# Kernel optimization log

Hardware: AMD Instinct MI355X
Metric: run time of the kernel (lower is better)

## Reference

```python
import jax, jax.numpy as jnp
import numpy as np

DN = ('NCDHW', 'OIDHW', 'NCDHW')
HEAD_COUNT = 8
LN_EPS = 1e-5


def _dwpw(x, dw_w, dw_b, pw_w, pw_b):
    # depthwise 3x3x3 conv (groups=C) followed by pointwise 1x1x1 conv, both with bias
    cin = x.shape[1]
    y = jax.lax.conv_general_dilated(x, dw_w, (1, 1, 1), [(1, 1), (1, 1), (1, 1)],
                                     dimension_numbers=DN, feature_group_count=cin)
    y = y + dw_b[None, :, None, None, None]
    y = jax.lax.conv_general_dilated(y, pw_w, (1, 1, 1), [(0, 0), (0, 0), (0, 0)],
                                     dimension_numbers=DN)
    return y + pw_b[None, :, None, None, None]


def setup_inputs() -> dict:
    key = jax.random.key(0)
    ks = iter(jax.random.split(key, 64))
    C, KC, VC = 256, 256, 256
    n, t, h, w = 4, 16, 28, 28
    d = {}
    d['input_rgb'] = jax.random.normal(next(ks), (n, C, t, h, w), dtype=jnp.float32)
    d['input_flow'] = jax.random.normal(next(ks), (n, C, t, h, w), dtype=jnp.float32)

    def conv_params(cin, cout, pfx):
        d[pfx + '_dw_w'] = jax.random.normal(next(ks), (cin, 1, 3, 3, 3), dtype=jnp.float32) * 0.05
        d[pfx + '_dw_b'] = jnp.zeros((cin,), dtype=jnp.float32)
        d[pfx + '_pw_w'] = jax.random.normal(next(ks), (cout, cin, 1, 1, 1), dtype=jnp.float32) * 0.05
        d[pfx + '_pw_b'] = jnp.zeros((cout,), dtype=jnp.float32)

    for s in ('rgb', 'flow'):
        for p, cout in (('k', KC), ('q', KC), ('v', VC)):
            conv_params(C, cout, f'{s}_{p}')
    conv_params(2 * VC, 2 * C, 'rp')
    return d


def reference(input_rgb, input_flow,
              rgb_k_dw_w, rgb_k_dw_b, rgb_k_pw_w, rgb_k_pw_b,
              rgb_q_dw_w, rgb_q_dw_b, rgb_q_pw_w, rgb_q_pw_b,
              rgb_v_dw_w, rgb_v_dw_b, rgb_v_pw_w, rgb_v_pw_b,
              flow_k_dw_w, flow_k_dw_b, flow_k_pw_w, flow_k_pw_b,
              flow_q_dw_w, flow_q_dw_b, flow_q_pw_w, flow_q_pw_b,
              flow_v_dw_w, flow_v_dw_b, flow_v_pw_w, flow_v_pw_b,
              rp_dw_w, rp_dw_b, rp_pw_w, rp_pw_b):
    n, C, t, h, w = input_rgb.shape
    S = t * h * w
    fused = jnp.concatenate([input_rgb, input_flow], axis=1)  # [n, 2C, t, h, w]

    def proj(x, dw_w, dw_b, pw_w, pw_b):
        return _dwpw(x, dw_w, dw_b, pw_w, pw_b).reshape(n, -1, S)

    keys = jnp.concatenate([proj(input_rgb, rgb_k_dw_w, rgb_k_dw_b, rgb_k_pw_w, rgb_k_pw_b),
                            proj(input_flow, flow_k_dw_w, flow_k_dw_b, flow_k_pw_w, flow_k_pw_b)], axis=1)
    queries = jnp.concatenate([proj(input_rgb, rgb_q_dw_w, rgb_q_dw_b, rgb_q_pw_w, rgb_q_pw_b),
                               proj(input_flow, flow_q_dw_w, flow_q_dw_b, flow_q_pw_w, flow_q_pw_b)], axis=1)
    values = jnp.concatenate([proj(input_rgb, rgb_v_dw_w, rgb_v_dw_b, rgb_v_pw_w, rgb_v_pw_b),
                              proj(input_flow, flow_v_dw_w, flow_v_dw_b, flow_v_pw_w, flow_v_pw_b)], axis=1)

    H = HEAD_COUNT
    hk = keys.shape[1] // H
    hv = values.shape[1] // H
    K = jax.nn.softmax(keys.reshape(n, H, hk, S), axis=3)      # softmax over sequence
    Q = jax.nn.softmax(queries.reshape(n, H, hk, S), axis=2)   # softmax over head channels
    V = values.reshape(n, H, hv, S)

    ctx = jnp.einsum('nhks,nhvs->nhkv', K, V)                   # [n,H,hk,hv]
    att = jnp.einsum('nhkv,nhks->nhvs', ctx, Q)                 # [n,H,hv,S]
    aggregated = att.reshape(n, H * hv, t, h, w)                # [n, 2*VC, t, h, w]

    rep = _dwpw(aggregated, rp_dw_w, rp_dw_b, rp_pw_w, rp_pw_b)
    x = rep + fused
    # f.layer_norm(x, x.size()): normalize over the ENTIRE tensor, no affine
    m = x.mean()
    v = x.var()
    return (x - m) / jnp.sqrt(v + LN_EPS)
```

## Files before the change

kernel.cpp:

```cpp
#include <hip/hip_runtime.h>
#include <math.h>


constexpr int NN = 4;
constexpr int C1 = 256;
constexpr int C2 = 512;
constexpr int TT = 16;
constexpr int SP = TT * 28 * 28;
constexpr long long NB = (long long)NN * C2 * SP;
constexpr int HEADS = 8;
constexpr int CTX_CHUNKS = 7;
constexpr int STATS_PARTS = 98 * 4 * 4;
constexpr double TOTAL_ELEMS = (double)NB;

typedef __attribute__((ext_vector_type(8))) short bf16x8;
typedef __attribute__((ext_vector_type(4))) short bf16x4;
typedef __attribute__((ext_vector_type(4))) float f32x4;

__device__ __forceinline__ short f2bf(float f)
{
    unsigned u = __float_as_uint(f);
    unsigned r = u + 0x7FFFu + ((u >> 16) & 1u);
    return (short)(r >> 16);
}
__device__ __forceinline__ float bf2f(short s)
{
    return __uint_as_float(((unsigned)(unsigned short)s) << 16);
}

__device__ __forceinline__ float4 loadvec4(const float* p)
{
    return *(const float4*)p;
}
__device__ __forceinline__ float4 loadvec4(const short* p)
{
    bf16x4 v = *(const bf16x4*)p;
    return (float4){bf2f(v[0]), bf2f(v[1]), bf2f(v[2]), bf2f(v[3])};
}

__device__ __forceinline__ void gload16(const short* g, short* l)
{
    __builtin_amdgcn_global_load_lds(
        (const __attribute__((address_space(1))) unsigned int*)g,
        (__attribute__((address_space(3))) unsigned int*)l,
        16, 0, 0);
}

__global__ __launch_bounds__(256)
void wcvt_kernel(const float* __restrict__ w0, const float* __restrict__ w1,
                 const float* __restrict__ w2, const float* __restrict__ w3,
                 const float* __restrict__ w4, const float* __restrict__ w5,
                 const float* __restrict__ w6, short* __restrict__ out)
{
    int i = blockIdx.x * 256 + threadIdx.x;
    if (i >= 655360) return;
    const float* src; int off;
    if (i < 393216) {
        int seg = i >> 16; off = i & 65535;
        src = seg == 0 ? w0 : seg == 1 ? w1 : seg == 2 ? w2
            : seg == 3 ? w3 : seg == 4 ? w4 : w5;
    } else { src = w6; off = i - 393216; }
    out[i] = f2bf(src[off]);
}

template<typename IT, int NSET>
__global__ __launch_bounds__(256)
void dwv_kernel(const IT* __restrict__ in,
                const float* __restrict__ w0c, const float* __restrict__ b0c,
                short* __restrict__ o0,
                const float* __restrict__ w1c, const float* __restrict__ b1c,
                short* __restrict__ o1,
                const float* __restrict__ w2c, const float* __restrict__ b2c,
                short* __restrict__ o2, int Cin)
{
    const int split = blockIdx.x, c = blockIdx.y, n = blockIdx.z;
    const int t0 = split * 8, t1 = t0 + 8;
    const int zs = (t0 - 1 > 0) ? t0 - 1 : 0;
    const int ze = (t1 < 15) ? t1 : 15;
    __shared__ float tile[2][900];
    const int tid = threadIdx.x;
    const size_t ibase = ((size_t)(n * Cin + c)) * TT * 784;
    const IT* inp = in + ibase;

    const float* wp[3] = {w0c, w1c, w2c};
    const float* bp[3] = {b0c, b1c, b2c};
    short* op[3] = {o0, o1, o2};
    float w[NSET][27], bv[NSET];
#pragma unroll
    for (int g = 0; g < NSET; ++g) {
#pragma unroll
        for (int i = 0; i < 27; ++i) w[g][i] = wp[g][c * 27 + i];
        bv[g] = bp[g][c];
    }

    for (int i = tid; i < 1800; i += 256) ((float*)tile)[i] = 0.f;

    const bool act = tid < 196;
    const int pos = tid * 4;
    const int hh = pos / 28, ww = pos - hh * 28;
    const int ladr = (hh + 1) * 30 + ww + 1;
    const int rbase = hh * 30 + ww;

    float4 preg = {0.f, 0.f, 0.f, 0.f};
    if (act) preg = loadvec4(inp + (size_t)zs * 784 + pos);

    float a0[NSET][4], a1[NSET][4], a2[NSET][4];
#pragma unroll
    for (int g = 0; g < NSET; ++g)
#pragma unroll
        for (int k = 0; k < 4; ++k) { a0[g][k] = bv[g]; a1[g][k] = bv[g]; a2[g][k] = bv[g]; }

    for (int z = zs; z <= ze; ++z) {
        float* tb = tile[z & 1];
        __syncthreads();
        if (act) {
            tb[ladr] = preg.x; tb[ladr + 1] = preg.y;
            tb[ladr + 2] = preg.z; tb[ladr + 3] = preg.w;
            if (z < ze) preg = loadvec4(inp + (size_t)(z + 1) * 784 + pos);
        }
        __syncthreads();
        if (act) {
            float v[3][6];
#pragma unroll
            for (int r = 0; r < 3; ++r)
#pragma unroll
                for (int j = 0; j < 6; ++j)
                    v[r][j] = tb[rbase + r * 30 + j];
#pragma unroll
            for (int g = 0; g < NSET; ++g)
#pragma unroll
                for (int dh = 0; dh < 3; ++dh)
#pragma unroll
                    for (int dw = 0; dw < 3; ++dw) {
                        const float wa = w[g][18 + dh * 3 + dw];
                        const float wb = w[g][9 + dh * 3 + dw];
                        const float wc2 = w[g][dh * 3 + dw];
#pragma unroll
                        for (int k = 0; k < 4; ++k) {
                            const float val = v[dh][k + dw];
                            a0[g][k] += val * wa;
                            a1[g][k] += val * wb;
                            a2[g][k] += val * wc2;
                        }
                    }
            if (z - 1 >= t0) {
#pragma unroll
                for (int g = 0; g < NSET; ++g) {
                    bf16x4 pk;
#pragma unroll
                    for (int k = 0; k < 4; ++k) pk[k] = f2bf(a0[g][k]);
                    *(bf16x4*)&op[g][ibase + (size_t)(z - 1) * 784 + pos] = pk;
                }
            }
#pragma unroll
            for (int g = 0; g < NSET; ++g)
#pragma unroll
                for (int k = 0; k < 4; ++k) {
                    a0[g][k] = a1[g][k]; a1[g][k] = a2[g][k]; a2[g][k] = bv[g];
                }
        }
    }
    if (act && ze >= t0 && ze < t1) {
#pragma unroll
        for (int g = 0; g < NSET; ++g) {
            bf16x4 pk;
#pragma unroll
            for (int k = 0; k < 4; ++k) pk[k] = f2bf(a0[g][k]);
            *(bf16x4*)&op[g][ibase + (size_t)ze * 784 + pos] = pk;
        }
    }
}

template<int MODE>
__global__ __launch_bounds__(256)
void pw_mfma_kernel(const short* __restrict__ Wb, const float* __restrict__ bias,
                    const short* __restrict__ act, short* __restrict__ outB,
                    float* __restrict__ outF, const float* __restrict__ rgb,
                    const float* __restrict__ flow, double* __restrict__ partials,
                    int Cin, size_t nStride, size_t cStride, int chOff)
{
    __shared__ short smem[17408];
    short* lA = smem;
    short* Bs = smem + 8192;
    const int tid = threadIdx.x;
    const int w = tid >> 6, lane = tid & 63;
    const int s0 = blockIdx.x * 128;
    const int m0 = blockIdx.y * 128;
    const int n = blockIdx.z;
    const short* aSrc = Wb + (size_t)m0 * Cin;
    const short* bSrc = act + (size_t)n * Cin * SP;
    f32x4 acc[4][4];
#pragma unroll
    for (int i = 0; i < 4; ++i)
#pragma unroll
        for (int j = 0; j < 4; ++j)
            acc[i][j] = (f32x4){0.f, 0.f, 0.f, 0.f};
    const int lrow = lane >> 3, lslot = lane & 7;
    const int wr = w >> 1, wc = w & 1;
    const int kg = tid >> 4, scb = tid & 15;

    for (int kt = 0; kt < Cin; kt += 64) {
#pragma unroll
        for (int cc = 0; cc < 4; ++cc) {
            const int chunk = w * 4 + cc;
            const int row = chunk * 8 + lrow;
            const int ss = lslot ^ (row & 7);
            gload16(aSrc + (size_t)row * Cin + kt + ss * 8, &lA[chunk * 512]);
        }
        bf16x8 breg[4];
#pragma unroll
        for (int r = 0; r < 4; ++r)
            breg[r] = *(const bf16x8*)(bSrc + (size_t)(kt + kg * 4 + r) * SP + s0 + scb * 8);
#pragma unroll
        for (int j = 0; j < 8; ++j) {
            bf16x4 pk;
#pragma unroll
            for (int r = 0; r < 4; ++r) pk[r] = breg[r][j];
            const int srow = scb * 8 + j;
            const int slot = (kg >> 1) ^ (scb & 7);
            *(bf16x4*)&Bs[srow * 72 + slot * 8 + (kg & 1) * 4] = pk;
        }
        __syncthreads();
#pragma unroll
        for (int kf = 0; kf < 2; ++kf) {
            bf16x8 af[4], bfr[4];
            const int kb = kf * 4 + (lane >> 4);
#pragma unroll
            for (int i = 0; i < 4; ++i) {
                const int row = wr * 64 + i * 16 + (lane & 15);
                af[i] = *(const bf16x8*)&lA[row * 64 + ((kb ^ (row & 7)) << 3)];
            }
#pragma unroll
            for (int j = 0; j < 4; ++j) {
                const int srow = wc * 64 + j * 16 + (lane & 15);
                bfr[j] = *(const bf16x8*)&Bs[srow * 72 + ((kb ^ ((srow >> 3) & 7)) << 3)];
            }
#pragma unroll
            for (int i = 0; i < 4; ++i)
#pragma unroll
                for (int j = 0; j < 4; ++j)
                    acc[i][j] = __builtin_amdgcn_mfma_f32_16x16x32_bf16(
                        af[i], bfr[j], acc[i][j], 0, 0, 0);
        }
        __syncthreads();
    }

    if constexpr (MODE == 0) {
        short* ep = smem;
#pragma unroll
        for (int i = 0; i < 4; ++i) {
            const int mloc = wr * 64 + i * 16 + (lane >> 4) * 4;
#pragma unroll
            for (int j = 0; j < 4; ++j) {
                const int sloc = wc * 64 + j * 16 + (lane & 15);
#pragma unroll
                for (int r = 0; r < 4; ++r)
                    ep[(mloc + r) * 136 + sloc] =
                        f2bf(acc[i][j][r] + bias[m0 + mloc + r]);
            }
        }
        __syncthreads();
        short* op = outB + (size_t)n * nStride;
#pragma unroll
        for (int cc = 0; cc < 8; ++cc) {
            const int idx = tid + cc * 256;
            const int mloc = idx >> 4, ch = idx & 15;
            bf16x8 v = *(const bf16x8*)&ep[mloc * 136 + ch * 8];
            *(bf16x8*)&op[(size_t)(chOff + m0 + mloc) * cStride + s0 + ch * 8] = v;
        }
    } else if constexpr (MODE == 1) {
        short* ep = smem;
#pragma unroll
        for (int i = 0; i < 4; ++i) {
            const int mb = wr * 64 + i * 16 + (lane >> 4) * 4;
#pragma unroll
            for (int j = 0; j < 4; ++j) {
                const int sloc = wc * 64 + j * 16 + (lane & 15);
                bf16x4 pk;
#pragma unroll
                for (int r = 0; r < 4; ++r)
                    pk[r] = f2bf(acc[i][j][r] + bias[m0 + mb + r]);
                *(bf16x4*)&ep[sloc * 136 + mb] = pk;
            }
        }
        __syncthreads();
#pragma unroll
        for (int cc = 0; cc < 8; ++cc) {
            const int idx = tid + cc * 256;
            const int sloc = idx >> 4, ch = idx & 15;
            bf16x8 v = *(const bf16x8*)&ep[sloc * 136 + ch * 8];
            *(bf16x8*)&outB[((size_t)n * SP + s0 + sloc) * 512 + chOff + m0 + ch * 8] = v;
        }
    } else {
        float* ep = (float*)smem;
        float* xp = outF + (size_t)n * C2 * SP;
        const float* rbase = (m0 < 256)
            ? rgb + ((size_t)n * 256 + m0) * SP
            : flow + ((size_t)n * 256 + (m0 - 256)) * SP;
        double ls = 0.0, lss = 0.0;
#pragma unroll
        for (int p = 0; p < 2; ++p) {
            if (p) __syncthreads();
            if (wr == p) {
#pragma unroll
                for (int i = 0; i < 4; ++i) {
                    const int mloc = i * 16 + (lane >> 4) * 4;
#pragma unroll
                    for (int j = 0; j < 4; ++j) {
                        const int sloc = wc * 64 + j * 16 + (lane & 15);
#pragma unroll
                        for (int r = 0; r < 4; ++r)
                            ep[(mloc + r) * 132 + sloc] =
                                acc[i][j][r] + bias[m0 + p * 64 + mloc + r];
                    }
                }
            }
            __syncthreads();
#pragma unroll
            for (int cc = 0; cc < 8; ++cc) {
                const int idx = tid + cc * 256;
                const int row = idx >> 5, ch = idx & 31;
                const int m = m0 + p * 64 + row;
                float4 a = *(const float4*)&ep[row * 132 + ch * 4];
                float4 rs = *(const float4*)&rbase[(size_t)(p * 64 + row) * SP + s0 + ch * 4];
                float4 x;
                x.x = a.x + rs.x; x.y = a.y + rs.y;
                x.z = a.z + rs.z; x.w = a.w + rs.w;
                *(float4*)&xp[(size_t)m * SP + s0 + ch * 4] = x;
                ls += (double)x.x + (double)x.y + (double)x.z + (double)x.w;
                lss += (double)x.x * x.x + (double)x.y * x.y +
                       (double)x.z * x.z + (double)x.w * x.w;
            }
        }
        __shared__ double s1[256], s2[256];
        s1[tid] = ls; s2[tid] = lss;
        __syncthreads();
        for (int st = 128; st > 0; st >>= 1) {
            if (tid < st) { s1[tid] += s1[tid + st]; s2[tid] += s2[tid + st]; }
            __syncthreads();
        }
        if (tid == 0) {
            const size_t bid = ((size_t)blockIdx.z * gridDim.y + blockIdx.y) *
                               gridDim.x + blockIdx.x;
            partials[2 * bid] = s1[0];
            partials[2 * bid + 1] = s2[0];
        }
    }
}

__global__ __launch_bounds__(256)
void row_stats_kernel(const short* __restrict__ K, float2* __restrict__ st)
{
    const short* p = K + (size_t)blockIdx.x * SP;
    __shared__ float sm[4];
    __shared__ float bc;
    const int tid = threadIdx.x, wv = tid >> 6, ln = tid & 63;
    float m = -1e30f;
    for (int c = tid; c < SP / 8; c += 256) {
        bf16x8 v = *(const bf16x8*)(p + c * 8);
#pragma unroll
        for (int j = 0; j < 8; ++j) m = fmaxf(m, bf2f(v[j]));
    }
    for (int o = 32; o; o >>= 1) m = fmaxf(m, __shfl_down(m, o, 64));
    if (ln == 0) sm[wv] = m;
    __syncthreads();
    if (tid == 0) bc = fmaxf(fmaxf(sm[0], sm[1]), fmaxf(sm[2], sm[3]));
    __syncthreads();
    m = bc;
    float sum = 0.f;
    for (int c = tid; c < SP / 8; c += 256) {
        bf16x8 v = *(const bf16x8*)(p + c * 8);
#pragma unroll
        for (int j = 0; j < 8; ++j) sum += __expf(bf2f(v[j]) - m);
    }
    for (int o = 32; o; o >>= 1) sum += __shfl_down(sum, o, 64);
    __syncthreads();
    if (ln == 0) sm[wv] = sum;
    __syncthreads();
    if (tid == 0) {
        float tot = sm[0] + sm[1] + sm[2] + sm[3];
        st[blockIdx.x] = (float2){m, 1.f / tot};
    }
}

__global__ __launch_bounds__(256)
void ctx_mfma_kernel(const short* __restrict__ Kb, const short* __restrict__ Vb,
                     const float2* __restrict__ stats, float* __restrict__ part)
{
    const int chunk = blockIdx.x, nh = blockIdx.y;
    const short* Kp = Kb + (size_t)nh * 64 * SP;
    const short* Vp = Vb + (size_t)nh * 64 * SP;
    __shared__ short lK[64 * 256];
    __shared__ short lV[64 * 256];
    const int tid = threadIdx.x;
    const int w = tid >> 6, lane = tid & 63;
    const int wr = w >> 1, wc = w & 1;
    f32x4 acc[2][2];
#pragma unroll
    for (int i = 0; i < 2; ++i)
#pragma unroll
        for (int j = 0; j < 2; ++j)
            acc[i][j] = (f32x4){0.f, 0.f, 0.f, 0.f};

    float km8[8], ki8[8];
#pragma unroll
    for (int ps = 0; ps < 8; ++ps) {
        float2 s = stats[nh * 64 + (tid >> 5) + ps * 8];
        km8[ps] = s.x; ki8[ps] = s.y;
    }

    for (int sub = 0; sub < 7; ++sub) {
        const int sOff = chunk * 1792 + sub * 256;
#pragma unroll
        for (int cc = 0; cc < 8; ++cc) {
            const int ch = w * 8 + cc;
            const int row = ch * 2 + (lane >> 5);
            const int sc = lane & 31;
            gload16(Vp + (size_t)row * SP + sOff + ((sc ^ (row & 7)) << 3),
                    &lV[ch * 512]);
        }
#pragma unroll
        for (int ps = 0; ps < 8; ++ps) {
            const int row = (tid >> 5) + ps * 8;
            const int sc = tid & 31;
            bf16x8 kv = *(const bf16x8*)(Kp + (size_t)row * SP + sOff + sc * 8);
            bf16x8 ev;
#pragma unroll
            for (int j = 0; j < 8; ++j)
                ev[j] = f2bf(__expf(bf2f(kv[j]) - km8[ps]) * ki8[ps]);
            *(bf16x8*)&lK[row * 256 + ((sc ^ (row & 7)) << 3)] = ev;
        }
        __syncthreads();
#pragma unroll
        for (int ks = 0; ks < 8; ++ks) {
            const int kb = ks * 4 + (lane >> 4);
            bf16x8 ak[2], bv[2];
#pragma unroll
            for (int i = 0; i < 2; ++i) {
                const int rk = wr * 32 + i * 16 + (lane & 15);
                ak[i] = *(const bf16x8*)&lK[rk * 256 + ((kb ^ (rk & 7)) << 3)];
            }
#pragma unroll
            for (int j = 0; j < 2; ++j) {
                const int rv = wc * 32 + j * 16 + (lane & 15);
                bv[j] = *(const bf16x8*)&lV[rv * 256 + ((kb ^ (rv & 7)) << 3)];
            }
#pragma unroll
            for (int i = 0; i < 2; ++i)
#pragma unroll
                for (int j = 0; j < 2; ++j)
                    acc[i][j] = __builtin_amdgcn_mfma_f32_16x16x32_bf16(
                        ak[i], bv[j], acc[i][j], 0, 0, 0);
        }
        __syncthreads();
    }
    float* op = part + ((size_t)nh * CTX_CHUNKS + chunk) * 4096;
#pragma unroll
    for (int i = 0; i < 2; ++i)
#pragma unroll
        for (int j = 0; j < 2; ++j)
#pragma unroll
            for (int r = 0; r < 4; ++r) {
                const int k = wr * 32 + i * 16 + (lane >> 4) * 4 + r;
                const int v = wc * 32 + j * 16 + (lane & 15);
                op[k * 64 + v] = acc[i][j][r];
            }
}

__global__ __launch_bounds__(256)
void ctx_reduce_kernel(const float* __restrict__ part, float* __restrict__ ctx)
{
    const int nh = blockIdx.x;
    for (int e = threadIdx.x; e < 4096; e += 256) {
        float s = 0.f;
        for (int c = 0; c < CTX_CHUNKS; ++c)
            s += part[((size_t)nh * CTX_CHUNKS + c) * 4096 + e];
        ctx[(size_t)nh * 4096 + e] = s;
    }
}

__global__ __launch_bounds__(256)
void att_kernel(const float* __restrict__ ctx, const short* __restrict__ Qb,
                short* __restrict__ out)
{
    const int nh = blockIdx.y;
    const int n = nh >> 3, h = nh & 7;
    const int s0 = blockIdx.x * 64;
    const float* cp = ctx + (size_t)nh * 4096;
    __shared__ short lC[64 * 64];
    __shared__ short lQ[64 * 64];
    __shared__ float red[64][4];
    __shared__ short lO[64 * 72];
    const int tid = threadIdx.x;
    const int w = tid >> 6, lane = tid & 63;

#pragma unroll
    for (int u = 0; u < 2; ++u) {
        const int si = (tid >> 6) + u * 4;
        const int v = tid & 63;
        bf16x8 pk;
#pragma unroll
        for (int j = 0; j < 8; ++j) pk[j] = f2bf(cp[(si * 8 + j) * 64 + v]);
        *(bf16x8*)&lC[v * 64 + ((si ^ (v & 7)) << 3)] = pk;
    }
    const int sq = tid >> 2, qpart = tid & 3;
    const short* Qrow = Qb + ((size_t)n * SP + s0 + sq) * 512 + h * 64 + qpart * 16;
    bf16x8 q0 = *(const bf16x8*)(Qrow);
    bf16x8 q1 = *(const bf16x8*)(Qrow + 8);
    float e[16];
    float mx = -1e30f;
#pragma unroll
    for (int j = 0; j < 8; ++j) {
        e[j] = bf2f(q0[j]); e[8 + j] = bf2f(q1[j]);
        mx = fmaxf(mx, fmaxf(e[j], e[8 + j]));
    }
    red[sq][qpart] = mx;
    __syncthreads();
    mx = fmaxf(fmaxf(red[sq][0], red[sq][1]), fmaxf(red[sq][2], red[sq][3]));
    float sum = 0.f;
#pragma unroll
    for (int j = 0; j < 16; ++j) { e[j] = __expf(e[j] - mx); sum += e[j]; }
    __syncthreads();
    red[sq][qpart] = sum;
    __syncthreads();
    const float sinv = 1.f / (red[sq][0] + red[sq][1] + red[sq][2] + red[sq][3]);
    bf16x8 p0, p1;
#pragma unroll
    for (int j = 0; j < 8; ++j) {
        p0[j] = f2bf(e[j] * sinv);
        p1[j] = f2bf(e[8 + j] * sinv);
    }
    *(bf16x8*)&lQ[sq * 64 + (((qpart * 2) ^ (sq & 7)) << 3)] = p0;
    *(bf16x8*)&lQ[sq * 64 + (((qpart * 2 + 1) ^ (sq & 7)) << 3)] = p1;
    __syncthreads();

    f32x4 acc[4];
#pragma unroll
    for (int i = 0; i < 4; ++i) acc[i] = (f32x4){0.f, 0.f, 0.f, 0.f};
    const int srow = w * 16 + (lane & 15);
#pragma unroll
    for (int ks = 0; ks < 2; ++ks) {
        const int kb = ks * 4 + (lane >> 4);
        bf16x8 bq = *(const bf16x8*)&lQ[srow * 64 + ((kb ^ (srow & 7)) << 3)];
#pragma unroll
        for (int i = 0; i < 4; ++i) {
            const int vr = i * 16 + (lane & 15);
            bf16x8 av = *(const bf16x8*)&lC[vr * 64 + ((kb ^ (vr & 7)) << 3)];
            acc[i] = __builtin_amdgcn_mfma_f32_16x16x32_bf16(av, bq, acc[i], 0, 0, 0);
        }
    }
#pragma unroll
    for (int i = 0; i < 4; ++i)
#pragma unroll
        for (int r = 0; r < 4; ++r)
            lO[(i * 16 + (lane >> 4) * 4 + r) * 72 + w * 16 + (lane & 15)] =
                f2bf(acc[i][r]);
    __syncthreads();
    short* op = out + (size_t)nh * 64 * SP;
#pragma unroll
    for (int cc = 0; cc < 2; ++cc) {
        const int idx = tid + cc * 256;
        const int v = idx >> 3, ch = idx & 7;
        bf16x8 t = *(const bf16x8*)&lO[v * 72 + ch * 8];
        *(bf16x8*)&op[(size_t)v * SP + s0 + ch * 8] = t;
    }
}

__global__ __launch_bounds__(256)
void stats_final_kernel(const double* __restrict__ partials, float* __restrict__ mv)
{
    double ls = 0.0, lss = 0.0;
    for (int i = threadIdx.x; i < STATS_PARTS; i += 256) {
        ls += partials[2 * i];
        lss += partials[2 * i + 1];
    }
    __shared__ double s1[256], s2[256];
    const int tid = threadIdx.x;
    s1[tid] = ls; s2[tid] = lss;
    __syncthreads();
    for (int s = 128; s > 0; s >>= 1) {
        if (tid < s) { s1[tid] += s1[tid + s]; s2[tid] += s2[tid + s]; }
        __syncthreads();
    }
    if (tid == 0) {
        double mean = s1[0] / TOTAL_ELEMS;
        double var = s2[0] / TOTAL_ELEMS - mean * mean;
        mv[0] = (float)mean;
        mv[1] = (float)(1.0 / sqrt(var + 1e-5));
    }
}

__global__ __launch_bounds__(256)
void normalize_kernel(float* __restrict__ x, const float* __restrict__ mv)
{
    const float mean = mv[0], inv = mv[1];
    size_t i = ((size_t)blockIdx.x * 256 + threadIdx.x) * 4;
    const size_t tot = (size_t)NB;
    const size_t step = (size_t)gridDim.x * 1024;
    for (; i < tot; i += step) {
        float4 v = *(float4*)&x[i];
        v.x = (v.x - mean) * inv; v.y = (v.y - mean) * inv;
        v.z = (v.z - mean) * inv; v.w = (v.w - mean) * inv;
        *(float4*)&x[i] = v;
    }
}

extern "C" void kernel_launch(void* const* d_in, const int* in_sizes, int n_in,
                              void* d_out, int out_size, void* d_ws, size_t ws_size,
                              hipStream_t stream)
{
    (void)in_sizes; (void)n_in; (void)out_size; (void)ws_size;
    const float* rgb = (const float*)d_in[0];
    const float* flow = (const float*)d_in[1];
    float* ws = (float*)d_ws;

    short* bufK = (short*)ws;
    short* bufQ = (short*)(ws + NB / 2);
    short* bufV = (short*)(ws + NB);
    short* actK = (short*)(ws + 3 * NB / 2);
    short* actQ = (short*)(ws + 7 * NB / 4);
    short* actV = (short*)(ws + 2 * NB);
    short* wB   = (short*)(ws + 9 * NB / 4);
    float2* rowStats = (float2*)(wB + 655360);
    float* ctxBuf = (float*)(rowStats + 2048);
    double* partials = (double*)(ctxBuf + 32 * 4096);
    float* mv = (float*)(partials + 2 * STATS_PARTS);
    float* ctxPart = ws + 3 * NB / 2;
    short* rpDw = actK;

    const size_t nsA = (size_t)C2 * SP, csA = SP;

    wcvt_kernel<<<2560, 256, 0, stream>>>(
        (const float*)d_in[4], (const float*)d_in[12], (const float*)d_in[16],
        (const float*)d_in[24], (const float*)d_in[8], (const float*)d_in[20],
        (const float*)d_in[28], wB);

    for (int st = 0; st < 2; ++st) {
        const float* src = st ? flow : rgb;
        const int kI = st ? 14 : 2, qI = st ? 18 : 6, vI = st ? 22 : 10;
        const int choff = st ? 256 : 0;
        dwv_kernel<float, 3><<<dim3(2, C1, NN), 256, 0, stream>>>(
            src,
            (const float*)d_in[kI], (const float*)d_in[kI + 1], actK,
            (const float*)d_in[qI], (const float*)d_in[qI + 1], actQ,
            (const float*)d_in[vI], (const float*)d_in[vI + 1], actV, C1);
        pw_mfma_kernel<0><<<dim3(SP / 128, 2, NN), 256, 0, stream>>>(
            wB + (size_t)(st ? 2 : 0) * 65536, (const float*)d_in[kI + 3], actK,
            bufK, nullptr, nullptr, nullptr, nullptr, C1, nsA, csA, choff);
        pw_mfma_kernel<0><<<dim3(SP / 128, 2, NN), 256, 0, stream>>>(
            wB + (size_t)(st ? 3 : 1) * 65536, (const float*)d_in[vI + 3], actV,
            bufV, nullptr, nullptr, nullptr, nullptr, C1, nsA, csA, choff);
        pw_mfma_kernel<1><<<dim3(SP / 128, 2, NN), 256, 0, stream>>>(
            wB + (size_t)(st ? 5 : 4) * 65536, (const float*)d_in[qI + 3], actQ,
            bufQ, nullptr, nullptr, nullptr, nullptr, C1, 0, 0, choff);
    }

    row_stats_kernel<<<NN * C2, 256, 0, stream>>>(bufK, rowStats);
    ctx_mfma_kernel<<<dim3(CTX_CHUNKS, NN * HEADS), 256, 0, stream>>>(
        bufK, bufV, rowStats, ctxPart);
    ctx_reduce_kernel<<<NN * HEADS, 256, 0, stream>>>(ctxPart, ctxBuf);
    att_kernel<<<dim3(SP / 64, NN * HEADS), 256, 0, stream>>>(
        ctxBuf, bufQ, bufV);

    dwv_kernel<short, 1><<<dim3(2, C2, NN), 256, 0, stream>>>(
        bufV, (const float*)d_in[26], (const float*)d_in[27], rpDw,
        nullptr, nullptr, nullptr, nullptr, nullptr, nullptr, C2);
    pw_mfma_kernel<2><<<dim3(SP / 128, 4, NN), 256, 0, stream>>>(
        wB + 6 * 65536, (const float*)d_in[29], rpDw, nullptr,
        (float*)d_out, rgb, flow, partials, C2, 0, 0, 0);

    stats_final_kernel<<<1, 256, 0, stream>>>(partials, mv);
    normalize_kernel<<<2048, 256, 0, stream>>>((float*)d_out, mv);
}
```

Before: 460.4 us.

## Double-buffer LDS tiles in pointwise MFMA GEMM to overlap loads with compute

Doubles the shared memory in the pointwise-conv MFMA kernel into two A/B stages. The next K-tile's global loads (async A loads into LDS, B loads into registers) are issued before the MFMAs on the current tile, and the B tile is transposed into LDS afterwards. The loop drops from two barriers per iteration to one. This hides global memory latency behind compute, at the cost of twice the LDS (about 68KB per block) and more registers, which may reduce occupancy.

```diff
diff --git a/kernel.cpp b/kernel.cpp
--- a/kernel.cpp
+++ b/kernel.cpp
@@ -179,9 +179,7 @@
                     const float* __restrict__ flow, double* __restrict__ partials,
                     int Cin, size_t nStride, size_t cStride, int chOff)
 {
-    __shared__ short smem[17408];
-    short* lA = smem;
-    short* Bs = smem + 8192;
+    __shared__ short smem[34816];
     const int tid = threadIdx.x;
     const int w = tid >> 6, lane = tid & 63;
     const int s0 = blockIdx.x * 128;
@@ -198,19 +196,22 @@
     const int lrow = lane >> 3, lslot = lane & 7;
     const int wr = w >> 1, wc = w & 1;
     const int kg = tid >> 4, scb = tid & 15;
-
-    for (int kt = 0; kt < Cin; kt += 64) {
+    const int nt = Cin >> 6;
+
+    {
+        short* nA = smem;
+        short* nB = smem + 16384;
 #pragma unroll
         for (int cc = 0; cc < 4; ++cc) {
             const int chunk = w * 4 + cc;
             const int row = chunk * 8 + lrow;
             const int ss = lslot ^ (row & 7);
-            gload16(aSrc + (size_t)row * Cin + kt + ss * 8, &lA[chunk * 512]);
+            gload16(aSrc + (size_t)row * Cin + ss * 8, &nA[chunk * 512]);
         }
         bf16x8 breg[4];
 #pragma unroll
         for (int r = 0; r < 4; ++r)
-            breg[r] = *(const bf16x8*)(bSrc + (size_t)(kt + kg * 4 + r) * SP + s0 + scb * 8);
+            breg[r] = *(const bf16x8*)(bSrc + (size_t)(kg * 4 + r) * SP + s0 + scb * 8);
 #pragma unroll
         for (int j = 0; j < 8; ++j) {
             bf16x4 pk;
@@ -218,9 +219,31 @@
             for (int r = 0; r < 4; ++r) pk[r] = breg[r][j];
             const int srow = scb * 8 + j;
             const int slot = (kg >> 1) ^ (scb & 7);
-            *(bf16x4*)&Bs[srow * 72 + slot * 8 + (kg & 1) * 4] = pk;
-        }
-        __syncthreads();
+            *(bf16x4*)&nB[srow * 72 + slot * 8 + (kg & 1) * 4] = pk;
+        }
+    }
+    __syncthreads();
+
+    for (int t = 0; t < nt; ++t) {
+        short* cA = smem + (t & 1) * 8192;
+        short* cB = smem + 16384 + (t & 1) * 9216;
+        short* nA = smem + ((t + 1) & 1) * 8192;
+        short* nB = smem + 16384 + ((t + 1) & 1) * 9216;
+        const bool more = (t + 1) < nt;
+        bf16x8 bnext[4];
+        if (more) {
+            const int kt = (t + 1) << 6;
+#pragma unroll
+            for (int cc = 0; cc < 4; ++cc) {
+                const int chunk = w * 4 + cc;
+                const int row = chunk * 8 + lrow;
+                const int ss = lslot ^ (row & 7);
+                gload16(aSrc + (size_t)row * Cin + kt + ss * 8, &nA[chunk * 512]);
+            }
+#pragma unroll
+            for (int r = 0; r < 4; ++r)
+                bnext[r] = *(const bf16x8*)(bSrc + (size_t)(kt + kg * 4 + r) * SP + s0 + scb * 8);
+        }
 #pragma unroll
         for (int kf = 0; kf < 2; ++kf) {
             bf16x8 af[4], bfr[4];
@@ -228,12 +251,12 @@
 #pragma unroll
             for (int i = 0; i < 4; ++i) {
                 const int row = wr * 64 + i * 16 + (lane & 15);
-                af[i] = *(const bf16x8*)&lA[row * 64 + ((kb ^ (row & 7)) << 3)];
+                af[i] = *(const bf16x8*)&cA[row * 64 + ((kb ^ (row & 7)) << 3)];
             }
 #pragma unroll
             for (int j = 0; j < 4; ++j) {
                 const int srow = wc * 64 + j * 16 + (lane & 15);
-                bfr[j] = *(const bf16x8*)&Bs[srow * 72 + ((kb ^ ((srow >> 3) & 7)) << 3)];
+                bfr[j] = *(const bf16x8*)&cB[srow * 72 + ((kb ^ ((srow >> 3) & 7)) << 3)];
             }
 #pragma unroll
             for (int i = 0; i < 4; ++i)
@@ -241,6 +264,17 @@
                 for (int j = 0; j < 4; ++j)
                     acc[i][j] = __builtin_amdgcn_mfma_f32_16x16x32_bf16(
                         af[i], bfr[j], acc[i][j], 0, 0, 0);
+        }
+        if (more) {
+#pragma unroll
+            for (int j = 0; j < 8; ++j) {
+                bf16x4 pk;
+#pragma unroll
+                for (int r = 0; r < 4; ++r) pk[r] = bnext[r][j];
+                const int srow = scb * 8 + j;
+                const int slot = (kg >> 1) ^ (scb & 7);
+                *(bf16x4*)&nB[srow * 72 + slot * 8 + (kg & 1) * 4] = pk;
+            }
         }
         __syncthreads();
     }
```

After: 443.7 us. 1.04x faster.
